# Performance work log

Hardware: AMD Instinct MI355X
Metric: run time of the kernel (lower is better)

## Reference

```python
import jax, jax.numpy as jnp
import numpy as np

P = 1048576   # total sampled points
N = 8192      # rays
E = 8         # experts
H = 128       # expert hidden dim
TOP_K = 2
INTERVAL = 0.5      # stepsize * voxel_size_ratio
ACT_SHIFT = -4.0    # models[-1].act_shift
THRESH = 1e-4       # fast_color_thres (ndc=False)


def raw2alpha(d):
    # Raw2Alpha: alpha = 1 - exp(-softplus(density + act_shift) * interval)
    return 1.0 - jnp.exp(-jax.nn.softplus(d + ACT_SHIFT) * INTERVAL)


def alphas2weights(alpha, ray_id, n_rays):
    # Sequential per-ray transmittance: w_j = alpha_j * prod_{k<j in ray}(1 - alpha_k)
    la = jnp.log1p(-jnp.clip(alpha, 0.0, 1.0 - 1e-6))      # [P], <= 0
    cum = jnp.cumsum(la)
    excl = cum - la                                          # exclusive cumsum, nonincreasing
    # offset per ray = excl at first point of the (sorted) segment == segment max
    offset = jax.ops.segment_max(excl, ray_id, num_segments=n_rays)
    T = jnp.exp(excl - offset[ray_id])                       # transmittance before each point
    weights = alpha * T
    alphainv_last = jnp.exp(jax.ops.segment_sum(la, ray_id, num_segments=n_rays))
    return weights, alphainv_last


def setup_inputs() -> dict:
    key = jax.random.key(0)
    ks = jax.random.split(key, 12)
    s = 0.3  # weight scale keeping activations in a sane range
    return {
        "ray_pts": jax.random.uniform(ks[0], (P, 3), dtype=jnp.float32),
        "viewdirs": jax.random.normal(ks[1], (N, 3), dtype=jnp.float32),
        "bg": jnp.ones((3,), dtype=jnp.float32),
        "Wd1": jax.random.normal(ks[2], (3, H), dtype=jnp.float32) * s,
        "bd1": jnp.zeros((H,), dtype=jnp.float32),
        "Wd2": jax.random.normal(ks[3], (H, 1), dtype=jnp.float32) * s,
        "Wg": jax.random.normal(ks[4], (6, E), dtype=jnp.float32) * s,
        "We1": jax.random.normal(ks[5], (E, 6, H), dtype=jnp.float32) * s,
        "be1": jnp.zeros((E, H), dtype=jnp.float32),
        "Wrgb": jax.random.normal(ks[6], (E, H, 3), dtype=jnp.float32) * s,
        "Walpha": jax.random.normal(ks[7], (E, H, 1), dtype=jnp.float32) * s,
        "ray_id": jnp.sort(jax.random.randint(ks[8], (P,), 0, N)).astype(jnp.int32),
    }


def reference(ray_pts, viewdirs, bg, Wd1, bd1, Wd2, Wg, We1, be1, Wrgb, Walpha, ray_id):
    # --- density grid query + activation ---
    hd = jax.nn.relu(ray_pts @ Wd1 + bd1)                    # [P,H]
    density = (hd @ Wd2)[:, 0]                               # [P]
    alpha0 = raw2alpha(density)
    # filter low density (zeroing alpha == dropping the point from the cumprod)
    alpha0 = jnp.where(alpha0 > THRESH, alpha0, 0.0)
    w0, _ = alphas2weights(alpha0, ray_id, N)
    # filter low transmittance (w0 <= THRESH also covers alpha0 == 0)
    keep = w0 > THRESH                                        # [P] bool

    # --- gate: softmax over experts, top-k, renormalize ---
    x = jnp.concatenate([ray_pts, viewdirs[ray_id]], axis=-1)  # [P,6]
    probs = jax.nn.softmax(x @ Wg, axis=-1)                    # [P,E]
    vals, idx = jax.lax.top_k(probs, TOP_K)                    # [P,K]
    vals = vals / jnp.sum(vals, axis=-1, keepdims=True)        # top_k > 1
    g = jnp.sum(vals[..., None] * jax.nn.one_hot(idx, E, dtype=vals.dtype), axis=1)  # [P,E]
    g = g * keep[:, None].astype(g.dtype)

    # --- per-expert radiance / alpha, mixed by gate weights ---
    rgb = jnp.zeros((ray_pts.shape[0], 3), dtype=ray_pts.dtype)
    alpha_mix = jnp.zeros((ray_pts.shape[0],), dtype=ray_pts.dtype)
    for e in range(E):  # fixed small expert count
        h = jax.nn.relu(x @ We1[e] + be1[e])                   # [P,H]
        rgb_e = jax.nn.sigmoid(h @ Wrgb[e])                    # [P,3]
        a_e = raw2alpha((h @ Walpha[e])[:, 0])                 # [P]
        rgb = rgb + g[:, e:e + 1] * rgb_e
        alpha_mix = alpha_mix + g[:, e] * a_e

    # --- composite: Alphas2Weights + segment_coo sum + background ---
    w, alphainv_last = alphas2weights(alpha_mix, ray_id, N)
    rgb_marched = jax.ops.segment_sum(w[:, None] * rgb, ray_id, num_segments=N)
    rgb_marched = rgb_marched + alphainv_last[:, None] * bg
    return rgb_marched
```

## Files before the change

kernel.cpp:

```cpp
#include <hip/hip_runtime.h>

#define PTOT   1048576
#define NRAYS  8192
#define THRESH 1e-4f

typedef float F2 __attribute__((ext_vector_type(2)));

__device__ __forceinline__ F2 f2splat(float s){ F2 r; r.x = s; r.y = s; return r; }
__device__ __forceinline__ F2 f2fma(F2 a, float b, F2 c){
    return __builtin_elementwise_fma(a, f2splat(b), c);
}

__device__ __forceinline__ float raw2alpha_f(float d){
    return 1.0f - rsqrtf(1.0f + __expf(d - 4.0f));
}

__global__ __launch_bounds__(256) void k_point(
    const float* __restrict__ pts, const float* __restrict__ vdirs,
    const int* __restrict__ ray_id,
    const float* __restrict__ Wd1, const float* __restrict__ bd1,
    const float* __restrict__ Wd2, const float* __restrict__ Wg,
    float* __restrict__ alpha0, float* __restrict__ g0a, int* __restrict__ eea)
{
    __shared__ float4 WD4[128];
    __shared__ float  WD2s[128];
    __shared__ float  WGs[8][6];
    int t = threadIdx.x;
    if (t < 128){
        WD4[t] = make_float4(Wd1[t], Wd1[128+t], Wd1[256+t], bd1[t]);
        WD2s[t] = Wd2[t];
    }
    if (t < 48) WGs[t & 7][t >> 3] = Wg[t];
    __syncthreads();

    int base = blockIdx.x * 2048 + t;
    F2 px[4], py[4], pz[4], vx[4], vy[4], vz[4], dens[4];
    #pragma unroll
    for (int q=0;q<4;q++){
        int p0 = base + (2*q)*256, p1 = p0 + 256;
        px[q] = (F2){pts[3*p0],   pts[3*p1]};
        py[q] = (F2){pts[3*p0+1], pts[3*p1+1]};
        pz[q] = (F2){pts[3*p0+2], pts[3*p1+2]};
        int r0 = ray_id[p0], r1 = ray_id[p1];
        vx[q] = (F2){vdirs[3*r0],   vdirs[3*r1]};
        vy[q] = (F2){vdirs[3*r0+1], vdirs[3*r1+1]};
        vz[q] = (F2){vdirs[3*r0+2], vdirs[3*r1+2]};
        dens[q] = f2splat(0.f);
    }
    #pragma unroll 2
    for (int i=0;i<128;i++){
        float4 w = WD4[i]; float w2 = WD2s[i];
        #pragma unroll
        for (int q=0;q<4;q++){
            F2 h = f2fma(px[q], w.x, f2fma(py[q], w.y, f2fma(pz[q], w.z, f2splat(w.w))));
            h = __builtin_elementwise_max(h, f2splat(0.f));
            dens[q] = f2fma(h, w2, dens[q]);
        }
    }
    #pragma unroll
    for (int q=0;q<4;q++){
        float a0 = raw2alpha_f(dens[q].x);
        float a1 = raw2alpha_f(dens[q].y);
        alpha0[base + (2*q)*256]   = (a0 > THRESH) ? a0 : 0.f;
        alpha0[base + (2*q+1)*256] = (a1 > THRESH) ? a1 : 0.f;
    }
    float m0[8], m1[8]; int i0[8], i1[8];
    #pragma unroll
    for (int j=0;j<8;j++){ m0[j]=-3.0e38f; m1[j]=-3.0e38f; i0[j]=0; i1[j]=0; }
    for (int e=0;e<8;e++){
        float w0=WGs[e][0],w1=WGs[e][1],w2=WGs[e][2],w3=WGs[e][3],w4=WGs[e][4],w5=WGs[e][5];
        #pragma unroll
        for (int q=0;q<4;q++){
            F2 l = f2fma(px[q],w0, f2fma(py[q],w1, f2fma(pz[q],w2,
                   f2fma(vx[q],w3, f2fma(vy[q],w4,
                   __builtin_elementwise_fma(vz[q], f2splat(w5), f2splat(0.f)))))));
            int j0 = 2*q, j1 = 2*q+1;
            float lx = l.x, ly = l.y;
            if (lx > m0[j0]){ m1[j0]=m0[j0]; i1[j0]=i0[j0]; m0[j0]=lx; i0[j0]=e; }
            else if (lx > m1[j0]){ m1[j0]=lx; i1[j0]=e; }
            if (ly > m0[j1]){ m1[j1]=m0[j1]; i1[j1]=i0[j1]; m0[j1]=ly; i0[j1]=e; }
            else if (ly > m1[j1]){ m1[j1]=ly; i1[j1]=e; }
        }
    }
    #pragma unroll
    for (int j=0;j<8;j++){
        float g0 = __fdividef(1.0f, 1.0f + __expf(m1[j]-m0[j]));
        g0a[base + j*256] = g0;
        eea[base + j*256] = i0[j] | (i1[j] << 8);
    }
}

__global__ __launch_bounds__(256) void k_rayoff(const int* __restrict__ ray_id,
                                                int* __restrict__ ray_off)
{
    int r = blockIdx.x*256 + threadIdx.x;
    if (r > NRAYS) return;
    int lo = 0, hi = PTOT;
    while (lo < hi){ int mid = (lo+hi) >> 1; if (ray_id[mid] < r) lo = mid+1; else hi = mid; }
    ray_off[r] = lo;
}

__global__ __launch_bounds__(256) void k_scan0(const float* __restrict__ alpha0,
                                               const int* __restrict__ eea,
                                               const int* __restrict__ ray_off,
                                               unsigned char* __restrict__ keep,
                                               int* __restrict__ cntA)
{
    __shared__ int wcs[4][8];
    int t = threadIdx.x, lane = t & 63, w = t >> 6;
    int wid = blockIdx.x*4 + w;
    int c[8];
    #pragma unroll
    for (int e=0;e<8;e++) c[e]=0;
    int s = ray_off[wid], e = ray_off[wid+1];
    float carry = 1.f;
    for (int ch = s; ch < e; ch += 64){
        int p = ch + lane;
        bool in = p < e;
        float a = in ? alpha0[p] : 0.f;
        int  ee = in ? eea[p] : 0;
        float incl = 1.f - a;
        #pragma unroll
        for (int d=1; d<64; d<<=1){ float tt = __shfl_up(incl, d); if (lane >= d) incl *= tt; }
        float excl = __shfl_up(incl, 1); if (lane == 0) excl = 1.f;
        float w0 = a * carry * excl;
        int k = (in && w0 > THRESH) ? 1 : 0;
        if (in) keep[p] = (unsigned char)k;
        int e0 = ee & 255, e1 = (ee >> 8) & 255;
        #pragma unroll
        for (int x=0;x<8;x++){
            unsigned long long m0 = __ballot(k && e0==x);
            unsigned long long m1 = __ballot(k && e1==x);
            c[x] += __popcll(m0) + __popcll(m1);
        }
        carry *= __shfl(incl, 63);
    }
    if (lane == 0){
        #pragma unroll
        for (int x=0;x<8;x++) wcs[w][x] = c[x];
    }
    __syncthreads();
    if (t < 8){
        int sum = wcs[0][t]+wcs[1][t]+wcs[2][t]+wcs[3][t];
        if (sum) atomicAdd(&cntA[t], sum);
    }
}

__global__ void k_offsets(const int* __restrict__ cntA,
                          int* __restrict__ offA, int* __restrict__ curA)
{
    if (threadIdx.x == 0 && blockIdx.x == 0){
        int acc = 0;
        for (int e = 0; e < 8; e++){ offA[e] = acc; acc += cntA[e]; curA[e] = 0; }
    }
}

__global__ __launch_bounds__(256) void k_fill(const unsigned char* __restrict__ keep,
                                              const float* __restrict__ g0a,
                                              const int* __restrict__ eea,
                                              const int* __restrict__ offA,
                                              int* __restrict__ curA,
                                              int2* __restrict__ ent)
{
    __shared__ int wc[4][8];
    __shared__ int wb[4][8];
    int t = threadIdx.x, lane = t & 63, w = t >> 6;
    unsigned long long lt = (1ull << lane) - 1ull;
    int base = blockIdx.x * 2048;

    int c[8];
    #pragma unroll
    for (int e=0;e<8;e++) c[e]=0;
    for (int j=0;j<8;j++){
        int p = base + (j*4 + w)*64 + lane;
        int k = keep[p];
        int ee = eea[p];
        int e0 = ee & 255, e1 = (ee >> 8) & 255;
        #pragma unroll
        for (int e=0;e<8;e++){
            unsigned long long m0 = __ballot(k && e0==e);
            unsigned long long m1 = __ballot(k && e1==e);
            c[e] += __popcll(m0) + __popcll(m1);
        }
    }
    if (lane == 0){
        #pragma unroll
        for (int e=0;e<8;e++) wc[w][e] = c[e];
    }
    __syncthreads();
    if (t < 8){
        int tot = wc[0][t]+wc[1][t]+wc[2][t]+wc[3][t];
        int b = offA[t] + (tot ? atomicAdd(&curA[t], tot) : 0);
        wb[0][t] = b; b += wc[0][t];
        wb[1][t] = b; b += wc[1][t];
        wb[2][t] = b; b += wc[2][t];
        wb[3][t] = b;
    }
    __syncthreads();

    int cur[8];
    #pragma unroll
    for (int e=0;e<8;e++) cur[e] = wb[w][e];
    for (int j=0;j<8;j++){
        int p = base + (j*4 + w)*64 + lane;
        int k = keep[p];
        float g0 = g0a[p];
        int ee = eea[p];
        int e0 = ee & 255, e1 = (ee >> 8) & 255;
        #pragma unroll
        for (int e=0;e<8;e++){
            unsigned long long m0 = __ballot(k && e0==e);
            unsigned long long m1 = __ballot(k && e1==e);
            if (k && e0==e)
                ent[cur[e] + __popcll(m0 & lt)] = make_int2(p, __float_as_int(g0));
            if (k && e1==e)
                ent[cur[e] + __popcll(m0) + __popcll(m1 & lt)] =
                    make_int2(p | (1 << 30), __float_as_int(1.0f - g0));
            cur[e] += __popcll(m0) + __popcll(m1);
        }
    }
}

__global__ __launch_bounds__(256) void k_expert(
    const int2* __restrict__ ent, const int* __restrict__ cntA,
    const int* __restrict__ offA,
    const float* __restrict__ pts, const float* __restrict__ vdirs,
    const int* __restrict__ ray_id,
    const float* __restrict__ We1, const float* __restrict__ be1,
    const float* __restrict__ Wrgb, const float* __restrict__ Walpha,
    float4* __restrict__ res)
{
    int e    = blockIdx.x >> 9;
    int bi   = blockIdx.x & 511;
    int n    = cntA[e];
    int base = bi * 2048;
    if (base >= n) return;

    __shared__ float4 WA[128];
    __shared__ float4 WB[128];
    __shared__ float4 WC[128];
    int t = threadIdx.x;
    if (t < 128){
        const float* w = We1 + e*768;
        WA[t] = make_float4(w[t], w[128+t], w[256+t], w[384+t]);
        WB[t] = make_float4(w[512+t], w[640+t], be1[e*128+t], Walpha[e*128+t]);
        const float* wr = Wrgb + e*384 + 3*t;
        WC[t] = make_float4(wr[0], wr[1], wr[2], 0.f);
    }
    __syncthreads();

    const int2* eb = ent + offA[e];
    F2 x0[4],x1[4],x2[4],x3[4],x4[4],x5[4];
    F2 ar[4],ag[4],ab[4],aa[4];
    #pragma unroll
    for (int pr=0;pr<4;pr++){
        int idx0 = base + t + (2*pr)*256, idx1 = idx0 + 256;
        int2 r0 = (idx0 < n) ? eb[idx0] : make_int2(0,0);
        int2 r1 = (idx1 < n) ? eb[idx1] : make_int2(0,0);
        int p0 = r0.x & 0x0FFFFFFF, p1 = r1.x & 0x0FFFFFFF;
        x0[pr] = (F2){pts[3*p0],   pts[3*p1]};
        x1[pr] = (F2){pts[3*p0+1], pts[3*p1+1]};
        x2[pr] = (F2){pts[3*p0+2], pts[3*p1+2]};
        int rd0 = ray_id[p0], rd1 = ray_id[p1];
        x3[pr] = (F2){vdirs[3*rd0],   vdirs[3*rd1]};
        x4[pr] = (F2){vdirs[3*rd0+1], vdirs[3*rd1+1]};
        x5[pr] = (F2){vdirs[3*rd0+2], vdirs[3*rd1+2]};
        ar[pr] = f2splat(0.f); ag[pr] = f2splat(0.f);
        ab[pr] = f2splat(0.f); aa[pr] = f2splat(0.f);
    }
    #pragma unroll 2
    for (int i=0;i<128;i++){
        float4 wa = WA[i], wb = WB[i], wc = WC[i];
        #pragma unroll
        for (int pr=0;pr<4;pr++){
            F2 h = f2fma(x0[pr],wa.x, f2fma(x1[pr],wa.y, f2fma(x2[pr],wa.z,
                   f2fma(x3[pr],wa.w, f2fma(x4[pr],wb.x, f2fma(x5[pr],wb.y,
                   f2splat(wb.z)))))));
            h = __builtin_elementwise_max(h, f2splat(0.f));
            ar[pr] = f2fma(h, wc.x, ar[pr]);
            ag[pr] = f2fma(h, wc.y, ag[pr]);
            ab[pr] = f2fma(h, wc.z, ab[pr]);
            aa[pr] = f2fma(h, wb.w, aa[pr]);
        }
    }
    #pragma unroll
    for (int pr=0;pr<4;pr++){
        #pragma unroll
        for (int sel=0; sel<2; sel++){
            int idx = base + t + (2*pr+sel)*256;
            if (idx < n){
                int2 rec = eb[idx];
                float vr = sel ? ar[pr].y : ar[pr].x;
                float vg = sel ? ag[pr].y : ag[pr].x;
                float vb = sel ? ab[pr].y : ab[pr].x;
                float va = sel ? aa[pr].y : aa[pr].x;
                float sr = __fdividef(1.0f, 1.0f + __expf(-vr));
                float sg = __fdividef(1.0f, 1.0f + __expf(-vg));
                float sb = __fdividef(1.0f, 1.0f + __expf(-vb));
                float a  = raw2alpha_f(va);
                float g  = __int_as_float(rec.y);
                int pp   = rec.x & 0x0FFFFFFF;
                int slot = ((unsigned)rec.x) >> 30;
                res[2*(size_t)pp + slot] = make_float4(g*sr, g*sg, g*sb, g*a);
            }
        }
    }
}

__global__ __launch_bounds__(256) void k_scan1(const float4* __restrict__ res,
                                               const unsigned char* __restrict__ keep,
                                               const int* __restrict__ ray_off,
                                               const float* __restrict__ bg,
                                               float* __restrict__ out)
{
    int wid  = (blockIdx.x*blockDim.x + threadIdx.x) >> 6;
    int lane = threadIdx.x & 63;
    if (wid >= NRAYS) return;
    int s = ray_off[wid], e = ray_off[wid+1];
    float carry = 1.f;
    float accx = 0.f, accy = 0.f, accz = 0.f;
    for (int c = s; c < e; c += 64){
        int p = c + lane;
        float4 v = make_float4(0.f,0.f,0.f,0.f);
        if (p < e && keep[p]){
            float4 v0 = res[2*(size_t)p];
            float4 v1 = res[2*(size_t)p + 1];
            v = make_float4(v0.x+v1.x, v0.y+v1.y, v0.z+v1.z, v0.w+v1.w);
        }
        float a = v.w;
        float incl = 1.f - a;
        #pragma unroll
        for (int d=1; d<64; d<<=1){ float tt = __shfl_up(incl, d); if (lane >= d) incl *= tt; }
        float excl = __shfl_up(incl, 1); if (lane == 0) excl = 1.f;
        float w = a * carry * excl;
        accx = fmaf(w, v.x, accx);
        accy = fmaf(w, v.y, accy);
        accz = fmaf(w, v.z, accz);
        carry *= __shfl(incl, 63);
    }
    #pragma unroll
    for (int d=32; d; d>>=1){
        accx += __shfl_xor(accx, d);
        accy += __shfl_xor(accy, d);
        accz += __shfl_xor(accz, d);
    }
    if (lane == 0){
        out[3*wid+0] = accx + carry*bg[0];
        out[3*wid+1] = accy + carry*bg[1];
        out[3*wid+2] = accz + carry*bg[2];
    }
}

extern "C" void kernel_launch(void* const* d_in, const int* in_sizes, int n_in,
                              void* d_out, int out_size, void* d_ws, size_t ws_size,
                              hipStream_t stream)
{
    const float* pts    = (const float*)d_in[0];
    const float* vdirs  = (const float*)d_in[1];
    const float* bg     = (const float*)d_in[2];
    const float* Wd1    = (const float*)d_in[3];
    const float* bd1    = (const float*)d_in[4];
    const float* Wd2    = (const float*)d_in[5];
    const float* Wg     = (const float*)d_in[6];
    const float* We1    = (const float*)d_in[7];
    const float* be1    = (const float*)d_in[8];
    const float* Wrgb   = (const float*)d_in[9];
    const float* Walpha = (const float*)d_in[10];
    const int*   ray_id = (const int*)d_in[11];
    float* out = (float*)d_out;

    char* ws = (char*)d_ws;
    size_t off = 0;
    float* alpha0        = (float*)(ws + off); off += (size_t)PTOT*4;
    float* g0a           = (float*)(ws + off); off += (size_t)PTOT*4;
    int*   eea           = (int*)  (ws + off); off += (size_t)PTOT*4;
    unsigned char* keep  = (unsigned char*)(ws + off); off += (size_t)PTOT;
    int*   ray_off       = (int*)  (ws + off); off += 65536;
    int*   cntA          = (int*)  (ws + off); off += 256;
    int*   offA          = (int*)  (ws + off); off += 256;
    int*   curA          = (int*)  (ws + off); off += 256;
    off = (off + 255) & ~(size_t)255;
    int2*  ent           = (int2*) (ws + off); off += (size_t)2*PTOT*8;
    float4* res          = (float4*)(ws + off); off += (size_t)2*PTOT*16;

    hipMemsetAsync(cntA, 0, 8*sizeof(int), stream);

    k_point  <<<PTOT/2048, 256, 0, stream>>>(pts, vdirs, ray_id, Wd1, bd1, Wd2, Wg,
                                             alpha0, g0a, eea);
    k_rayoff <<<(NRAYS+256)/256, 256, 0, stream>>>(ray_id, ray_off);
    k_scan0  <<<NRAYS/4, 256, 0, stream>>>(alpha0, eea, ray_off, keep, cntA);
    k_offsets<<<1, 64, 0, stream>>>(cntA, offA, curA);
    k_fill   <<<PTOT/2048, 256, 0, stream>>>(keep, g0a, eea, offA, curA, ent);
    k_expert <<<8*512, 256, 0, stream>>>(ent, cntA, offA, pts, vdirs, ray_id,
                                         We1, be1, Wrgb, Walpha, res);
    k_scan1  <<<NRAYS*64/256, 256, 0, stream>>>(res, keep, ray_off, bg, out);
}
```

Baseline: 251.8 us.

## Run expert MLP on bf16 MFMA with pre-packed point features

```diff
diff --git a/kernel.cpp b/kernel.cpp
--- a/kernel.cpp
+++ b/kernel.cpp
@@ -1,26 +1,34 @@
 #include <hip/hip_runtime.h>
+#include <hip/hip_bf16.h>
 
 #define PTOT   1048576
 #define NRAYS  8192
 #define THRESH 1e-4f
 
-typedef float F2 __attribute__((ext_vector_type(2)));
+typedef float F2  __attribute__((ext_vector_type(2)));
+typedef short S8  __attribute__((ext_vector_type(8)));
+typedef float F4v __attribute__((ext_vector_type(4)));
 
 __device__ __forceinline__ F2 f2splat(float s){ F2 r; r.x = s; r.y = s; return r; }
 __device__ __forceinline__ F2 f2fma(F2 a, float b, F2 c){
     return __builtin_elementwise_fma(a, f2splat(b), c);
 }
-
 __device__ __forceinline__ float raw2alpha_f(float d){
     return 1.0f - rsqrtf(1.0f + __expf(d - 4.0f));
 }
+__device__ __forceinline__ unsigned f2bf(float f){
+    unsigned u = __float_as_uint(f);
+    return (u + 0x7FFFu + ((u >> 16) & 1u)) >> 16;
+}
+union HB2 { __hip_bfloat162 h; unsigned u; };
 
 __global__ __launch_bounds__(256) void k_point(
     const float* __restrict__ pts, const float* __restrict__ vdirs,
     const int* __restrict__ ray_id,
     const float* __restrict__ Wd1, const float* __restrict__ bd1,
     const float* __restrict__ Wd2, const float* __restrict__ Wg,
-    float* __restrict__ alpha0, float* __restrict__ g0a, int* __restrict__ eea)
+    float* __restrict__ alpha0, float* __restrict__ g0a, int* __restrict__ eea,
+    int4* __restrict__ xq)
 {
     __shared__ float4 WD4[128];
     __shared__ float  WD2s[128];
@@ -64,6 +72,20 @@
         alpha0[base + (2*q)*256]   = (a0 > THRESH) ? a0 : 0.f;
         alpha0[base + (2*q+1)*256] = (a1 > THRESH) ? a1 : 0.f;
     }
+    #pragma unroll
+    for (int q=0;q<4;q++){
+        #pragma unroll
+        for (int s=0;s<2;s++){
+            float fx = s? px[q].y:px[q].x, fy = s? py[q].y:py[q].x, fz = s? pz[q].y:pz[q].x;
+            float gx = s? vx[q].y:vx[q].x, gy = s? vy[q].y:vy[q].x, gz = s? vz[q].y:vz[q].x;
+            int4 v;
+            v.x = (int)(f2bf(fx) | (f2bf(fy) << 16));
+            v.y = (int)(f2bf(fz) | (f2bf(gx) << 16));
+            v.z = (int)(f2bf(gy) | (f2bf(gz) << 16));
+            v.w = (int)0x3F80u;
+            xq[base + (2*q+s)*256] = v;
+        }
+    }
     float m0[8], m1[8]; int i0[8], i1[8];
     #pragma unroll
     for (int j=0;j<8;j++){ m0[j]=-3.0e38f; m1[j]=-3.0e38f; i0[j]=0; i1[j]=0; }
@@ -223,85 +245,99 @@
 
 __global__ __launch_bounds__(256) void k_expert(
     const int2* __restrict__ ent, const int* __restrict__ cntA,
-    const int* __restrict__ offA,
-    const float* __restrict__ pts, const float* __restrict__ vdirs,
-    const int* __restrict__ ray_id,
+    const int* __restrict__ offA, const int4* __restrict__ xq,
     const float* __restrict__ We1, const float* __restrict__ be1,
     const float* __restrict__ Wrgb, const float* __restrict__ Walpha,
-    float4* __restrict__ res)
-{
-    int e    = blockIdx.x >> 9;
-    int bi   = blockIdx.x & 511;
+    float* __restrict__ resf)
+{
+    int e    = blockIdx.x >> 10;
+    int bi   = blockIdx.x & 1023;
     int n    = cntA[e];
-    int base = bi * 2048;
+    int base = bi * 1024;
     if (base >= n) return;
-
-    __shared__ float4 WA[128];
-    __shared__ float4 WB[128];
-    __shared__ float4 WC[128];
-    int t = threadIdx.x;
-    if (t < 128){
-        const float* w = We1 + e*768;
-        WA[t] = make_float4(w[t], w[128+t], w[256+t], w[384+t]);
-        WB[t] = make_float4(w[512+t], w[640+t], be1[e*128+t], Walpha[e*128+t]);
-        const float* wr = Wrgb + e*384 + 3*t;
-        WC[t] = make_float4(wr[0], wr[1], wr[2], 0.f);
-    }
-    __syncthreads();
-
+    int t = threadIdx.x, lane = t & 63, w = t >> 6;
+    int c16 = lane & 15, quad = lane >> 4;
     const int2* eb = ent + offA[e];
-    F2 x0[4],x1[4],x2[4],x3[4],x4[4],x5[4];
-    F2 ar[4],ag[4],ab[4],aa[4];
-    #pragma unroll
-    for (int pr=0;pr<4;pr++){
-        int idx0 = base + t + (2*pr)*256, idx1 = idx0 + 256;
-        int2 r0 = (idx0 < n) ? eb[idx0] : make_int2(0,0);
-        int2 r1 = (idx1 < n) ? eb[idx1] : make_int2(0,0);
-        int p0 = r0.x & 0x0FFFFFFF, p1 = r1.x & 0x0FFFFFFF;
-        x0[pr] = (F2){pts[3*p0],   pts[3*p1]};
-        x1[pr] = (F2){pts[3*p0+1], pts[3*p1+1]};
-        x2[pr] = (F2){pts[3*p0+2], pts[3*p1+2]};
-        int rd0 = ray_id[p0], rd1 = ray_id[p1];
-        x3[pr] = (F2){vdirs[3*rd0],   vdirs[3*rd1]};
-        x4[pr] = (F2){vdirs[3*rd0+1], vdirs[3*rd1+1]};
-        x5[pr] = (F2){vdirs[3*rd0+2], vdirs[3*rd1+2]};
-        ar[pr] = f2splat(0.f); ag[pr] = f2splat(0.f);
-        ab[pr] = f2splat(0.f); aa[pr] = f2splat(0.f);
-    }
-    #pragma unroll 2
-    for (int i=0;i<128;i++){
-        float4 wa = WA[i], wb = WB[i], wc = WC[i];
-        #pragma unroll
-        for (int pr=0;pr<4;pr++){
-            F2 h = f2fma(x0[pr],wa.x, f2fma(x1[pr],wa.y, f2fma(x2[pr],wa.z,
-                   f2fma(x3[pr],wa.w, f2fma(x4[pr],wb.x, f2fma(x5[pr],wb.y,
-                   f2splat(wb.z)))))));
-            h = __builtin_elementwise_max(h, f2splat(0.f));
-            ar[pr] = f2fma(h, wc.x, ar[pr]);
-            ag[pr] = f2fma(h, wc.y, ag[pr]);
-            ab[pr] = f2fma(h, wc.z, ab[pr]);
-            aa[pr] = f2fma(h, wb.w, aa[pr]);
-        }
-    }
-    #pragma unroll
-    for (int pr=0;pr<4;pr++){
-        #pragma unroll
-        for (int sel=0; sel<2; sel++){
-            int idx = base + t + (2*pr+sel)*256;
-            if (idx < n){
-                int2 rec = eb[idx];
-                float vr = sel ? ar[pr].y : ar[pr].x;
-                float vg = sel ? ag[pr].y : ag[pr].x;
-                float vb = sel ? ab[pr].y : ab[pr].x;
-                float va = sel ? aa[pr].y : aa[pr].x;
-                float sr = __fdividef(1.0f, 1.0f + __expf(-vr));
-                float sg = __fdividef(1.0f, 1.0f + __expf(-vg));
-                float sb = __fdividef(1.0f, 1.0f + __expf(-vb));
-                float a  = raw2alpha_f(va);
-                float g  = __int_as_float(rec.y);
-                int pp   = rec.x & 0x0FFFFFFF;
-                int slot = ((unsigned)rec.x) >> 30;
-                res[2*(size_t)pp + slot] = make_float4(g*sr, g*sg, g*sb, g*a);
+
+    S8 A1[8];
+    #pragma unroll
+    for (int mt=0; mt<8; mt++){
+        S8 f = (S8)0;
+        if (quad == 0){
+            int hid = mt*16 + c16;
+            #pragma unroll
+            for (int j=0;j<6;j++) f[j] = (short)f2bf(We1[e*768 + j*128 + hid]);
+            f[6] = (short)f2bf(be1[e*128 + hid]);
+        }
+        A1[mt] = f;
+    }
+    S8 B2[4];
+    #pragma unroll
+    for (int s=0;s<4;s++){
+        S8 f = (S8)0;
+        if (c16 < 4){
+            #pragma unroll
+            for (int j=0;j<8;j++){
+                int k2 = s*32 + quad*8 + j;
+                float v = (c16 < 3) ? Wrgb[e*384 + k2*3 + c16] : Walpha[e*128 + k2];
+                f[j] = (short)f2bf(v);
+            }
+        }
+        B2[s] = f;
+    }
+
+    __shared__ short Hlds[4][16][136];
+    short* hbase = &Hlds[w][0][0];
+    const F4v zf = {0.f, 0.f, 0.f, 0.f};
+
+    for (int chunk = 0; chunk < 4; chunk++){
+        int cbase = base + w*256 + chunk*64;
+        if (cbase >= n) break;
+        int idx = cbase + lane;
+        int2 rec = (idx < n) ? eb[idx] : make_int2(PTOT, 0);
+        int4 xv  = xq[rec.x & 0x0FFFFFFF];
+        float g  = __int_as_float(rec.y);
+
+        #pragma unroll
+        for (int t4=0; t4<4; t4++){
+            int src = t4*16 + c16;
+            union { int4 i; S8 s; } bu;
+            bu.i.x = __shfl(xv.x, src); bu.i.y = __shfl(xv.y, src);
+            bu.i.z = __shfl(xv.z, src); bu.i.w = __shfl(xv.w, src);
+            S8 bfrag = (quad == 0) ? bu.s : (S8)0;
+
+            #pragma unroll
+            for (int mt=0; mt<8; mt++){
+                F4v h = __builtin_amdgcn_mfma_f32_16x16x32_bf16(A1[mt], bfrag, zf, 0, 0, 0);
+                HB2 p0, p1;
+                p0.h = __float22bfloat162_rn(make_float2(fmaxf(h[0],0.f), fmaxf(h[1],0.f)));
+                p1.h = __float22bfloat162_rn(make_float2(fmaxf(h[2],0.f), fmaxf(h[3],0.f)));
+                int ofs = c16*136 + mt*16 + quad*4;
+                *(int2*)(hbase + ofs) = make_int2((int)p0.u, (int)p1.u);
+            }
+            F4v o = zf;
+            #pragma unroll
+            for (int s=0;s<4;s++){
+                S8 a2 = *(const S8*)(hbase + c16*136 + s*32 + quad*8);
+                o = __builtin_amdgcn_mfma_f32_16x16x32_bf16(a2, B2[s], o, 0, 0, 0);
+            }
+            float ge[4]; int pe[4];
+            #pragma unroll
+            for (int r=0;r<4;r++){
+                int elane = t4*16 + quad*4 + r;
+                ge[r] = __shfl(g, elane);
+                pe[r] = __shfl(rec.x, elane);
+            }
+            if (c16 < 4){
+                #pragma unroll
+                for (int r=0;r<4;r++){
+                    float v = o[r];
+                    float outv = (c16 == 3) ? raw2alpha_f(v)
+                               : __fdividef(1.0f, 1.0f + __expf(-v));
+                    int pp = pe[r] & 0x0FFFFFFF;
+                    int sl = ((unsigned)pe[r]) >> 30;
+                    resf[(size_t)(2*pp + sl)*4 + c16] = ge[r] * outv;
+                }
             }
         }
     }
@@ -380,18 +416,19 @@
     int*   offA          = (int*)  (ws + off); off += 256;
     int*   curA          = (int*)  (ws + off); off += 256;
     off = (off + 255) & ~(size_t)255;
+    int4*  xq            = (int4*) (ws + off); off += ((size_t)PTOT+1)*16;
     int2*  ent           = (int2*) (ws + off); off += (size_t)2*PTOT*8;
-    float4* res          = (float4*)(ws + off); off += (size_t)2*PTOT*16;
+    float4* res          = (float4*)(ws + off); off += ((size_t)2*PTOT+2)*16;
 
     hipMemsetAsync(cntA, 0, 8*sizeof(int), stream);
 
     k_point  <<<PTOT/2048, 256, 0, stream>>>(pts, vdirs, ray_id, Wd1, bd1, Wd2, Wg,
-                                             alpha0, g0a, eea);
+                                             alpha0, g0a, eea, xq);
     k_rayoff <<<(NRAYS+256)/256, 256, 0, stream>>>(ray_id, ray_off);
     k_scan0  <<<NRAYS/4, 256, 0, stream>>>(alpha0, eea, ray_off, keep, cntA);
     k_offsets<<<1, 64, 0, stream>>>(cntA, offA, curA);
     k_fill   <<<PTOT/2048, 256, 0, stream>>>(keep, g0a, eea, offA, curA, ent);
-    k_expert <<<8*512, 256, 0, stream>>>(ent, cntA, offA, pts, vdirs, ray_id,
-                                         We1, be1, Wrgb, Walpha, res);
+    k_expert <<<8*1024, 256, 0, stream>>>(ent, cntA, offA, xq,
+                                          We1, be1, Wrgb, Walpha, (float*)res);
     k_scan1  <<<NRAYS*64/256, 256, 0, stream>>>(res, keep, ray_off, bg, out);
 }
```

New measurement: 264.8 us. 1.05x slower.

## Fold ray offsets and expert offsets into neighbouring kernels, cache per-point viewdirs

Applied to the files above, without the earlier changes.

```diff
diff --git a/kernel.cpp b/kernel.cpp
--- a/kernel.cpp
+++ b/kernel.cpp
@@ -10,7 +10,6 @@
 __device__ __forceinline__ F2 f2fma(F2 a, float b, F2 c){
     return __builtin_elementwise_fma(a, f2splat(b), c);
 }
-
 __device__ __forceinline__ float raw2alpha_f(float d){
     return 1.0f - rsqrtf(1.0f + __expf(d - 4.0f));
 }
@@ -20,7 +19,8 @@
     const int* __restrict__ ray_id,
     const float* __restrict__ Wd1, const float* __restrict__ bd1,
     const float* __restrict__ Wd2, const float* __restrict__ Wg,
-    float* __restrict__ alpha0, float* __restrict__ g0a, int* __restrict__ eea)
+    float* __restrict__ alpha0, float* __restrict__ g0a, int* __restrict__ eea,
+    float4* __restrict__ vd, int* __restrict__ ray_off)
 {
     __shared__ float4 WD4[128];
     __shared__ float  WD2s[128];
@@ -35,6 +35,7 @@
 
     int base = blockIdx.x * 2048 + t;
     F2 px[4], py[4], pz[4], vx[4], vy[4], vz[4], dens[4];
+    int rid0[4], rid1[4];
     #pragma unroll
     for (int q=0;q<4;q++){
         int p0 = base + (2*q)*256, p1 = p0 + 256;
@@ -42,10 +43,22 @@
         py[q] = (F2){pts[3*p0+1], pts[3*p1+1]};
         pz[q] = (F2){pts[3*p0+2], pts[3*p1+2]};
         int r0 = ray_id[p0], r1 = ray_id[p1];
+        rid0[q] = r0; rid1[q] = r1;
         vx[q] = (F2){vdirs[3*r0],   vdirs[3*r1]};
         vy[q] = (F2){vdirs[3*r0+1], vdirs[3*r1+1]};
         vz[q] = (F2){vdirs[3*r0+2], vdirs[3*r1+2]};
         dens[q] = f2splat(0.f);
+    }
+    #pragma unroll
+    for (int q=0;q<4;q++){
+        int p0 = base + (2*q)*256, p1 = p0 + 256;
+        vd[p0] = make_float4(vx[q].x, vy[q].x, vz[q].x, 0.f);
+        vd[p1] = make_float4(vx[q].y, vy[q].y, vz[q].y, 0.f);
+        int prev0 = (p0 == 0) ? -1 : ray_id[p0-1];
+        if (prev0 != rid0[q]) for (int r=prev0+1; r<=rid0[q]; ++r) ray_off[r] = p0;
+        int prev1 = ray_id[p1-1];
+        if (prev1 != rid1[q]) for (int r=prev1+1; r<=rid1[q]; ++r) ray_off[r] = p1;
+        if (p1 == PTOT-1) for (int r=rid1[q]+1; r<=NRAYS; ++r) ray_off[r] = PTOT;
     }
     #pragma unroll 2
     for (int i=0;i<128;i++){
@@ -90,16 +103,6 @@
     }
 }
 
-__global__ __launch_bounds__(256) void k_rayoff(const int* __restrict__ ray_id,
-                                                int* __restrict__ ray_off)
-{
-    int r = blockIdx.x*256 + threadIdx.x;
-    if (r > NRAYS) return;
-    int lo = 0, hi = PTOT;
-    while (lo < hi){ int mid = (lo+hi) >> 1; if (ray_id[mid] < r) lo = mid+1; else hi = mid; }
-    ray_off[r] = lo;
-}
-
 __global__ __launch_bounds__(256) void k_scan0(const float* __restrict__ alpha0,
                                                const int* __restrict__ eea,
                                                const int* __restrict__ ray_off,
@@ -146,24 +149,16 @@
     }
 }
 
-__global__ void k_offsets(const int* __restrict__ cntA,
-                          int* __restrict__ offA, int* __restrict__ curA)
-{
-    if (threadIdx.x == 0 && blockIdx.x == 0){
-        int acc = 0;
-        for (int e = 0; e < 8; e++){ offA[e] = acc; acc += cntA[e]; curA[e] = 0; }
-    }
-}
-
 __global__ __launch_bounds__(256) void k_fill(const unsigned char* __restrict__ keep,
                                               const float* __restrict__ g0a,
                                               const int* __restrict__ eea,
-                                              const int* __restrict__ offA,
+                                              const int* __restrict__ cntA,
                                               int* __restrict__ curA,
                                               int2* __restrict__ ent)
 {
     __shared__ int wc[4][8];
     __shared__ int wb[4][8];
+    __shared__ int sOff[8];
     int t = threadIdx.x, lane = t & 63, w = t >> 6;
     unsigned long long lt = (1ull << lane) - 1ull;
     int base = blockIdx.x * 2048;
@@ -187,10 +182,14 @@
         #pragma unroll
         for (int e=0;e<8;e++) wc[w][e] = c[e];
     }
+    if (t == 0){
+        int acc = 0;
+        for (int e=0;e<8;e++){ sOff[e] = acc; acc += cntA[e]; }
+    }
     __syncthreads();
     if (t < 8){
         int tot = wc[0][t]+wc[1][t]+wc[2][t]+wc[3][t];
-        int b = offA[t] + (tot ? atomicAdd(&curA[t], tot) : 0);
+        int b = sOff[t] + (tot ? atomicAdd(&curA[t], tot) : 0);
         wb[0][t] = b; b += wc[0][t];
         wb[1][t] = b; b += wc[1][t];
         wb[2][t] = b; b += wc[2][t];
@@ -223,22 +222,19 @@
 
 __global__ __launch_bounds__(256) void k_expert(
     const int2* __restrict__ ent, const int* __restrict__ cntA,
-    const int* __restrict__ offA,
-    const float* __restrict__ pts, const float* __restrict__ vdirs,
-    const int* __restrict__ ray_id,
+    const float* __restrict__ pts, const float4* __restrict__ vd,
     const float* __restrict__ We1, const float* __restrict__ be1,
     const float* __restrict__ Wrgb, const float* __restrict__ Walpha,
     float4* __restrict__ res)
 {
     int e    = blockIdx.x >> 9;
     int bi   = blockIdx.x & 511;
-    int n    = cntA[e];
     int base = bi * 2048;
-    if (base >= n) return;
 
     __shared__ float4 WA[128];
     __shared__ float4 WB[128];
     __shared__ float4 WC[128];
+    __shared__ int sSeg[2];
     int t = threadIdx.x;
     if (t < 128){
         const float* w = We1 + e*768;
@@ -247,9 +243,16 @@
         const float* wr = Wrgb + e*384 + 3*t;
         WC[t] = make_float4(wr[0], wr[1], wr[2], 0.f);
     }
-    __syncthreads();
-
-    const int2* eb = ent + offA[e];
+    if (t == 0){
+        int acc = 0;
+        for (int i=0;i<e;i++) acc += cntA[i];
+        sSeg[0] = acc; sSeg[1] = cntA[e];
+    }
+    __syncthreads();
+    int n = sSeg[1];
+    if (base >= n) return;
+    const int2* eb = ent + sSeg[0];
+
     F2 x0[4],x1[4],x2[4],x3[4],x4[4],x5[4];
     F2 ar[4],ag[4],ab[4],aa[4];
     #pragma unroll
@@ -261,10 +264,10 @@
         x0[pr] = (F2){pts[3*p0],   pts[3*p1]};
         x1[pr] = (F2){pts[3*p0+1], pts[3*p1+1]};
         x2[pr] = (F2){pts[3*p0+2], pts[3*p1+2]};
-        int rd0 = ray_id[p0], rd1 = ray_id[p1];
-        x3[pr] = (F2){vdirs[3*rd0],   vdirs[3*rd1]};
-        x4[pr] = (F2){vdirs[3*rd0+1], vdirs[3*rd1+1]};
-        x5[pr] = (F2){vdirs[3*rd0+2], vdirs[3*rd1+2]};
+        float4 v0 = vd[p0], v1 = vd[p1];
+        x3[pr] = (F2){v0.x, v1.x};
+        x4[pr] = (F2){v0.y, v1.y};
+        x5[pr] = (F2){v0.z, v1.z};
         ar[pr] = f2splat(0.f); ag[pr] = f2splat(0.f);
         ab[pr] = f2splat(0.f); aa[pr] = f2splat(0.f);
     }
@@ -375,23 +378,21 @@
     float* g0a           = (float*)(ws + off); off += (size_t)PTOT*4;
     int*   eea           = (int*)  (ws + off); off += (size_t)PTOT*4;
     unsigned char* keep  = (unsigned char*)(ws + off); off += (size_t)PTOT;
-    int*   ray_off       = (int*)  (ws + off); off += 65536;
+    int*   ray_off       = (int*)  (ws + off); off += 33024;
     int*   cntA          = (int*)  (ws + off); off += 256;
-    int*   offA          = (int*)  (ws + off); off += 256;
     int*   curA          = (int*)  (ws + off); off += 256;
     off = (off + 255) & ~(size_t)255;
+    float4* vd           = (float4*)(ws + off); off += (size_t)PTOT*16;
     int2*  ent           = (int2*) (ws + off); off += (size_t)2*PTOT*8;
-    float4* res          = (float4*)(ws + off); off += (size_t)2*PTOT*16;
-
-    hipMemsetAsync(cntA, 0, 8*sizeof(int), stream);
-
-    k_point  <<<PTOT/2048, 256, 0, stream>>>(pts, vdirs, ray_id, Wd1, bd1, Wd2, Wg,
-                                             alpha0, g0a, eea);
-    k_rayoff <<<(NRAYS+256)/256, 256, 0, stream>>>(ray_id, ray_off);
-    k_scan0  <<<NRAYS/4, 256, 0, stream>>>(alpha0, eea, ray_off, keep, cntA);
-    k_offsets<<<1, 64, 0, stream>>>(cntA, offA, curA);
-    k_fill   <<<PTOT/2048, 256, 0, stream>>>(keep, g0a, eea, offA, curA, ent);
-    k_expert <<<8*512, 256, 0, stream>>>(ent, cntA, offA, pts, vdirs, ray_id,
-                                         We1, be1, Wrgb, Walpha, res);
-    k_scan1  <<<NRAYS*64/256, 256, 0, stream>>>(res, keep, ray_off, bg, out);
-}
+    float4* res          = (float4*)(ws + off); off += ((size_t)2*PTOT+2)*16;
+
+    hipMemsetAsync(cntA, 0, 512, stream);
+
+    k_point <<<PTOT/2048, 256, 0, stream>>>(pts, vdirs, ray_id, Wd1, bd1, Wd2, Wg,
+                                            alpha0, g0a, eea, vd, ray_off);
+    k_scan0 <<<NRAYS/4, 256, 0, stream>>>(alpha0, eea, ray_off, keep, cntA);
+    k_fill  <<<PTOT/2048, 256, 0, stream>>>(keep, g0a, eea, cntA, curA, ent);
+    k_expert<<<8*512, 256, 0, stream>>>(ent, cntA, pts, vd,
+                                        We1, be1, Wrgb, Walpha, res);
+    k_scan1 <<<NRAYS*64/256, 256, 0, stream>>>(res, keep, ray_off, bg, out);
+}
```

After: 249.1 us. No clear change (-1.1%).
